# Optimization experiments

Measured on AMD Instinct MI355X. Metric: run time of the kernel, lower is better.

Reference implementation:

```python
import jax, jax.numpy as jnp
import numpy as np

B, N, C, H, D, K = 8, 2000, 64, 64, 16, 2  # batch, nodes, hidden, hidden_hidden, embed_dim, cheb_k


def setup_inputs() -> dict:
    key = jax.random.key(0)
    ks = jax.random.split(key, 12)
    f = lambda k, s, sc=1.0: jax.random.normal(k, s, dtype=jnp.float32) * sc
    return {
        "z": f(ks[0], (B, N, C)),
        "W_in": f(ks[1], (H, C), 0.1),
        "b_in": f(ks[2], (H,), 0.1),
        "W_out": f(ks[3], (C * C, H), 0.05),
        "b_out": f(ks[4], (C * C,), 0.05),
        "emb": f(ks[5], (N, D), 0.1),
        "wp": f(ks[6], (D, K, H, H), 0.1),
        "bp": f(ks[7], (D, H), 0.1),
        "w1": f(ks[8], (C,)),
        "w2": f(ks[9], (C,)),
        "vs": f(ks[10], (N, N), 0.02),
        "bs": f(ks[11], (N, N), 0.02),
    }


def reference(z, W_in, b_in, W_out, b_out, emb, wp, bp, w1, w2, vs, bs):
    # linear_in + relu: (B,N,C) -> (B,N,H)
    h = jax.nn.relu(jnp.einsum("bnc,hc->bnh", z, W_in) + b_in)

    # data-adaptive graph: softmax over rows of relu(emb @ emb^T)
    A = jax.nn.softmax(jax.nn.relu(emb @ emb.T), axis=1)  # (N,N)
    S = jnp.stack([jnp.eye(N, dtype=z.dtype), A], axis=0)  # (K,N,N), cheb_k=2

    # spatial attention on h (x = h.unsqueeze(1), f_in == H == C)
    e1 = h @ w1  # (B,N)
    e2 = h @ w2  # (B,N)
    prod = e1[:, :, None] * e2[:, None, :]  # (B,N,N) outer product
    E = jax.nn.softmax(
        jnp.einsum("nm,bmp->bnp", vs, jax.nn.sigmoid(prod + bs)), axis=-1
    )  # (B,N,N)

    # batched supports: E.unsqueeze(1) @ S -> (B,K,N,N)
    sup = jnp.einsum("bnm,kmp->bknp", E, S)

    # node-adaptive weights / bias
    weights = jnp.einsum("nd,dkio->nkio", emb, wp)  # (N,K,H,H)
    bias = emb @ bp  # (N,H)

    # graph conv
    x_g = jnp.einsum("bknm,bmc->bnkc", sup, h)  # (B,N,K,H)
    g = jnp.einsum("bnki,nkio->bno", x_g, weights) + bias  # (B,N,H)

    # linear_out + view + tanh, scaled by 0.1
    out = jnp.tanh(jnp.einsum("bnh,oh->bno", g, W_out) + b_out)
    return 0.1 * out.reshape(B, N, C, C)
```

## Files before the change

### kernel.cpp

```cpp
#include <hip/hip_runtime.h>
#include <hip/hip_bf16.h>

#define NN 2000
#define NP 2048
#define BB 8
#define HH 64
#define DD 16

typedef __hip_bfloat16 bf16;
typedef short bf16x8 __attribute__((ext_vector_type(8)));
typedef float f32x4 __attribute__((ext_vector_type(4)));

__device__ __forceinline__ float fast_sigmoid(float x) {
    return 1.0f / (1.0f + __expf(-x));
}
__device__ __forceinline__ float fast_tanh(float x) {
    float e = __expf(2.0f * x);
    return 1.0f - 2.0f / (e + 1.0f);
}

__device__ __forceinline__ void glds16(const void* g, void* l) {
    __builtin_amdgcn_global_load_lds(
        (const __attribute__((address_space(1))) void*)g,
        (__attribute__((address_space(3))) void*)l, 16, 0, 0);
}

__global__ __launch_bounds__(256) void k_h(
        const float* __restrict__ z, const float* __restrict__ W_in,
        const float* __restrict__ b_in, const float* __restrict__ w1,
        const float* __restrict__ w2, float* __restrict__ h,
        float* __restrict__ e1, float* __restrict__ e2) {
    __shared__ float WT[64 * 65];
    __shared__ float zs[4][64];
    int t = threadIdx.x;
    int lane = t & 63, ty = t >> 6;
    int bn0 = blockIdx.x * 4;
    for (int i = t; i < 64 * 64; i += 256) {
        int hh = i >> 6, c = i & 63;
        WT[c * 65 + hh] = W_in[i];
    }
    zs[ty][lane] = z[(size_t)(bn0 + ty) * 64 + lane];
    __syncthreads();
    float acc = b_in[lane];
    #pragma unroll
    for (int c = 0; c < 64; c++) acc += zs[ty][c] * WT[c * 65 + lane];
    float hv = fmaxf(acc, 0.0f);
    h[(size_t)(bn0 + ty) * 64 + lane] = hv;
    float p1 = hv * w1[lane], p2 = hv * w2[lane];
    #pragma unroll
    for (int off = 32; off > 0; off >>= 1) {
        p1 += __shfl_down(p1, off);
        p2 += __shfl_down(p2, off);
    }
    if (lane == 0) { e1[bn0 + ty] = p1; e2[bn0 + ty] = p2; }
}

__global__ __launch_bounds__(256) void k_A(const float* __restrict__ emb,
                                           bf16* __restrict__ A) {
    int i = blockIdx.x, t = threadIdx.x;
    if (i >= NN) {
        for (int j = t; j < NP; j += 256) A[(size_t)i * NP + j] = __float2bfloat16(0.0f);
        return;
    }
    __shared__ float ei[DD];
    __shared__ float rowbuf[NP];
    __shared__ float red[256];
    if (t < DD) ei[t] = emb[i * DD + t];
    __syncthreads();
    float lmax = -1e30f;
    for (int j = t; j < NP; j += 256) {
        float s = 0.0f;
        if (j < NN) {
            #pragma unroll
            for (int d = 0; d < DD; d++) s += ei[d] * emb[j * DD + d];
            s = fmaxf(s, 0.0f);
            lmax = fmaxf(lmax, s);
        }
        rowbuf[j] = s;
    }
    red[t] = lmax; __syncthreads();
    for (int o = 128; o > 0; o >>= 1) { if (t < o) red[t] = fmaxf(red[t], red[t + o]); __syncthreads(); }
    float mx = red[0];
    __syncthreads();
    float lsum = 0.0f;
    for (int j = t; j < NN; j += 256) {
        float e = __expf(rowbuf[j] - mx);
        rowbuf[j] = e; lsum += e;
    }
    red[t] = lsum; __syncthreads();
    for (int o = 128; o > 0; o >>= 1) { if (t < o) red[t] += red[t + o]; __syncthreads(); }
    float inv = 1.0f / red[0];
    for (int j = t; j < NP; j += 256)
        A[(size_t)i * NP + j] = __float2bfloat16(j < NN ? rowbuf[j] * inv : 0.0f);
}

__global__ void k_cvt_vs(const float* __restrict__ vs, bf16* __restrict__ out) {
    int id = blockIdx.x * 256 + threadIdx.x;
    int n = id >> 11, m = id & (NP - 1);
    float v = (n < NN && m < NN) ? vs[n * NN + m] : 0.0f;
    out[id] = __float2bfloat16(v);
}

__global__ void k_cvt_wout(const float* __restrict__ W_out, bf16* __restrict__ out) {
    int id = blockIdx.x * 256 + threadIdx.x;
    out[id] = __float2bfloat16(W_out[id]);
}

__global__ __launch_bounds__(256) void k_wn(const float* __restrict__ emb,
                                            const float* __restrict__ wp,
                                            float* __restrict__ Wn_all) {
    __shared__ float embs[128 * 16];
    int t = threadIdx.x;
    int n0 = blockIdx.x * 128;
    int jo = blockIdx.y * 256 + t;
    float wv[16];
    #pragma unroll
    for (int d = 0; d < 16; d++) wv[d] = wp[(size_t)d * 8192 + jo];
    for (int s = t; s < 128 * 16; s += 256) {
        int i = s >> 4, d = s & 15;
        int n = n0 + i;
        embs[s] = (n < NN) ? emb[n * 16 + d] : 0.f;
    }
    __syncthreads();
    for (int i = 0; i < 128; i++) {
        int n = n0 + i;
        if (n >= NN) break;
        const f32x4* ev = (const f32x4*)&embs[i * 16];
        f32x4 e0 = ev[0], e1 = ev[1], e2 = ev[2], e3 = ev[3];
        float a = 0.f;
        #pragma unroll
        for (int q = 0; q < 4; q++) a += e0[q] * wv[q];
        #pragma unroll
        for (int q = 0; q < 4; q++) a += e1[q] * wv[4 + q];
        #pragma unroll
        for (int q = 0; q < 4; q++) a += e2[q] * wv[8 + q];
        #pragma unroll
        for (int q = 0; q < 4; q++) a += e3[q] * wv[12 + q];
        Wn_all[(size_t)n * 8192 + jo] = a;
    }
}

__global__ __launch_bounds__(256) void k_hT(const float* __restrict__ h,
                                            bf16* __restrict__ hTcat,
                                            bf16* __restrict__ hsT) {
    __shared__ float tile[64 * 65];
    int nt = blockIdx.x, b = blockIdx.y;
    int tx = threadIdx.x & 63, ty = threadIdx.x >> 6;
    int n0 = nt * 64;
    for (int i = ty * 16; i < ty * 16 + 16; i++) {
        int n = n0 + i;
        tile[i * 65 + tx] = (n < NN) ? h[((size_t)b * NN + n) * 64 + tx] : 0.0f;
    }
    __syncthreads();
    for (int i = ty * 16; i < ty * 16 + 16; i++) {
        bf16 v = __float2bfloat16(tile[tx * 65 + i]);
        hTcat[((size_t)b * 64 + i) * NP + n0 + tx] = v;
        hsT[((size_t)b * 128 + i) * NP + n0 + tx] = v;
    }
}

__global__ __launch_bounds__(256) void k_AhT(const float* __restrict__ Ahcat,
                                             bf16* __restrict__ hsT) {
    __shared__ float tile[64 * 65];
    int pt = blockIdx.x, b = blockIdx.y;
    int tx = threadIdx.x & 63, ty = threadIdx.x >> 6;
    int p0 = pt * 64, q0 = b * 64;
    for (int i = ty * 16; i < ty * 16 + 16; i++)
        tile[i * 65 + tx] = Ahcat[((size_t)p0 + i) * 512 + q0 + tx];
    __syncthreads();
    for (int i = ty * 16; i < ty * 16 + 16; i++)
        hsT[((size_t)b * 128 + 64 + i) * NP + p0 + tx] =
            __float2bfloat16(tile[tx * 65 + i]);
}

__global__ __launch_bounds__(256) void k_Tt(const float* __restrict__ e1,
                                            const float* __restrict__ e2,
                                            const float* __restrict__ bs,
                                            bf16* __restrict__ Tt) {
    __shared__ float tile[64 * 65];
    int b = blockIdx.z;
    e1 += (size_t)b * NN;
    e2 += (size_t)b * NN;
    Tt += (size_t)b * NP * NP;
    int mt = blockIdx.x, pt = blockIdx.y;
    int tx = threadIdx.x & 63, ty = threadIdx.x >> 6;
    int m0 = mt * 64, p0 = pt * 64;
    int p = p0 + tx;
    float e2v = (p < NN) ? e2[p] : 0.0f;
    for (int i = ty * 16; i < ty * 16 + 16; i++) {
        int m = m0 + i;
        float v = 0.0f;
        if (m < NN && p < NN)
            v = fast_sigmoid(e1[m] * e2v + bs[(size_t)m * NN + p]);
        tile[i * 65 + tx] = v;
    }
    __syncthreads();
    for (int i = ty * 16; i < ty * 16 + 16; i++)
        Tt[((size_t)p0 + i) * NP + m0 + tx] = __float2bfloat16(tile[tx * 65 + i]);
}

__global__ __launch_bounds__(512) void k_gemm256p(
        const bf16* __restrict__ X, const bf16* __restrict__ Yt,
        bf16* __restrict__ P, float* __restrict__ rowsumP,
        int K, int ldx, int ldy,
        long long sY, long long sP) {
    __shared__ short As[2 * 256 * 64];
    __shared__ short Bs[2 * 256 * 64];
    __shared__ float rsum2[4][256];
    int z = blockIdx.z;
    const bf16* Xp = X;
    const bf16* Yp = Yt + (long long)z * sY;
    bf16* Pp = P + (long long)z * sP;
    int tid = threadIdx.x;
    int m0 = blockIdx.x * 256, n0 = blockIdx.y * 256;
    int wave = tid >> 6, lane = tid & 63;
    int wr = wave >> 2, wc = wave & 3;
    int fr = lane & 15, kq = lane >> 4;

    f32x4 zero = {0.f, 0.f, 0.f, 0.f};
    f32x4 acc[8][4];
    #pragma unroll
    for (int i = 0; i < 8; i++)
        #pragma unroll
        for (int j = 0; j < 4; j++) acc[i][j] = zero;

    int r8 = tid >> 3;
    int sslot = (tid & 7) ^ (r8 & 7);
    const bf16* xsrc = Xp + (long long)(m0 + r8) * ldx + sslot * 8;
    const bf16* ysrc = Yp + (long long)(n0 + r8) * ldy + sslot * 8;

    auto STAGE = [&](int tile) {
        short* Ab = As + (tile & 1) * 16384 + tid * 8;
        short* Bb = Bs + (tile & 1) * 16384 + tid * 8;
        int ko = tile * 64;
        #pragma unroll
        for (int c = 0; c < 4; c++) {
            glds16(xsrc + (long long)(c * 64) * ldx + ko, Ab + c * 4096);
            glds16(ysrc + (long long)(c * 64) * ldy + ko, Bb + c * 4096);
        }
    };

    int NT = K >> 6;
    STAGE(0);
    STAGE(1);
    asm volatile("s_waitcnt vmcnt(8)" ::: "memory");
    __builtin_amdgcn_s_barrier();

    for (int t = 0; t < NT; t++) {
        const short* Ab = As + (t & 1) * 16384 + wr * 8192 + fr * 64;
        const short* Bb = Bs + (t & 1) * 16384 + wc * 4096 + fr * 64;
        #pragma unroll
        for (int ks = 0; ks < 2; ks++) {
            int s = ((ks * 4 + kq) ^ (fr & 7)) * 8;
            bf16x8 a[8], b[4];
            #pragma unroll
            for (int i = 0; i < 8; i++)
                a[i] = *(const bf16x8*)(Ab + i * 1024 + s);
            #pragma unroll
            for (int j = 0; j < 4; j++)
                b[j] = *(const bf16x8*)(Bb + j * 1024 + s);
            __builtin_amdgcn_s_setprio(1);
            #pragma unroll
            for (int i = 0; i < 8; i++)
                #pragma unroll
                for (int j = 0; j < 4; j++)
                    acc[i][j] = __builtin_amdgcn_mfma_f32_16x16x32_bf16(a[i], b[j], acc[i][j], 0, 0, 0);
            __builtin_amdgcn_s_setprio(0);
        }
        __builtin_amdgcn_sched_barrier(0);
        __builtin_amdgcn_s_barrier();
        __builtin_amdgcn_sched_barrier(0);
        if (t + 2 < NT) {
            STAGE(t + 2);
            asm volatile("s_waitcnt vmcnt(8)" ::: "memory");
            __builtin_amdgcn_s_barrier();
        } else if (t + 1 < NT) {
            asm volatile("s_waitcnt vmcnt(0)" ::: "memory");
            __builtin_amdgcn_s_barrier();
        }
    }

    int rq = kq * 4;
    #pragma unroll
    for (int i = 0; i < 8; i++) {
        #pragma unroll
        for (int r = 0; r < 4; r++) {
            int lrow = wr * 128 + i * 16 + rq + r;
            long long grow = m0 + lrow;
            float rs = 0.f;
            #pragma unroll
            for (int j = 0; j < 4; j++) {
                int col = n0 + wc * 64 + j * 16 + fr;
                float e = (col < NN) ? __expf(acc[i][j][r]) : 0.f;
                Pp[grow * (long long)NP + col] = __float2bfloat16(e);
                rs += e;
            }
            rs += __shfl_xor(rs, 1);
            rs += __shfl_xor(rs, 2);
            rs += __shfl_xor(rs, 4);
            rs += __shfl_xor(rs, 8);
            if (fr == 0) rsum2[wc][lrow] = rs;
        }
    }
    __syncthreads();
    if (tid < 256) {
        float s = rsum2[0][tid] + rsum2[1][tid] + rsum2[2][tid] + rsum2[3][tid];
        rowsumP[((long long)z * 8 + blockIdx.y) * NP + m0 + tid] = s;
    }
}

template<bool TANH, int KSPLIT>
__global__ __launch_bounds__(256) void k_gemm_bt(
        const bf16* __restrict__ X, const bf16* __restrict__ Yt,
        float* __restrict__ C, const float* __restrict__ bias,
        int K, int ldx, int ldy, int ldc,
        long long sX, long long sY, long long sC, long long sSlice) {
    __shared__ short As[128 * 32];
    __shared__ short Bs[128 * 32];
    int zz = blockIdx.z;
    int ks = 0;
    if (KSPLIT > 1) { ks = zz % KSPLIT; zz /= KSPLIT; }
    const bf16* Xp = X + (long long)zz * sX;
    const bf16* Yp = Yt + (long long)zz * sY;
    float* Cp = C + (long long)zz * sC + (long long)ks * sSlice;
    int tid = threadIdx.x;
    int m0 = blockIdx.x * 128, n0 = blockIdx.y * 128;
    int wave = tid >> 6, lane = tid & 63;
    int wm = (wave >> 1) * 64, wn = (wave & 1) * 64;
    int fr = lane & 15, kq = lane >> 4;

    f32x4 zero = {0.f, 0.f, 0.f, 0.f};
    f32x4 acc[4][4];
    #pragma unroll
    for (int i = 0; i < 4; i++)
        #pragma unroll
        for (int j = 0; j < 4; j++) acc[i][j] = zero;

    int lrow = lane >> 2, lcol = (lane & 3) * 8;
    const bf16* xg0 = Xp + (long long)(m0 + wave * 16 + lrow) * ldx + lcol;
    const bf16* xg1 = xg0 + (long long)64 * ldx;
    const bf16* yg0 = Yp + (long long)(n0 + wave * 16 + lrow) * ldy + lcol;
    const bf16* yg1 = yg0 + (long long)64 * ldy;
    short* lA0 = As + wave * 512;
    short* lA1 = As + (wave + 4) * 512;
    short* lB0 = Bs + wave * 512;
    short* lB1 = Bs + (wave + 4) * 512;

    int kbeg = (KSPLIT > 1) ? ks * (K / KSPLIT) : 0;
    int kend = kbeg + K / KSPLIT;
    for (int k0 = kbeg; k0 < kend; k0 += 32) {
        __syncthreads();
        glds16(xg0 + k0, lA0);
        glds16(xg1 + k0, lA1);
        glds16(yg0 + k0, lB0);
        glds16(yg1 + k0, lB1);
        __syncthreads();
        bf16x8 a[4], b[4];
        #pragma unroll
        for (int i = 0; i < 4; i++)
            a[i] = *(const bf16x8*)(As + (wm + i * 16 + fr) * 32 + kq * 8);
        #pragma unroll
        for (int j = 0; j < 4; j++)
            b[j] = *(const bf16x8*)(Bs + (wn + j * 16 + fr) * 32 + kq * 8);
        #pragma unroll
        for (int i = 0; i < 4; i++)
            #pragma unroll
            for (int j = 0; j < 4; j++)
                acc[i][j] = __builtin_amdgcn_mfma_f32_16x16x32_bf16(a[i], b[j], acc[i][j], 0, 0, 0);
    }
    int rq = kq * 4;
    for (int i = 0; i < 4; i++)
        for (int j = 0; j < 4; j++) {
            int col = n0 + wn + j * 16 + fr;
            float bv = TANH ? bias[col] : 0.0f;
            #pragma unroll
            for (int r = 0; r < 4; r++) {
                int row = m0 + wm + i * 16 + rq + r;
                float v = acc[i][j][r];
                Cp[(long long)row * ldc + col] =
                    TANH ? 0.1f * fast_tanh(v + bv) : v;
            }
        }
}

__global__ __launch_bounds__(256) void k_reduce4(const float* __restrict__ part,
                                                 float* __restrict__ out, int total) {
    int i = (blockIdx.x * 256 + threadIdx.x) * 4;
    f32x4 a = *(const f32x4*)(part + i);
    f32x4 b = *(const f32x4*)(part + (size_t)total + i);
    f32x4 c = *(const f32x4*)(part + (size_t)2 * total + i);
    f32x4 d = *(const f32x4*)(part + (size_t)3 * total + i);
    *(f32x4*)(out + i) = (a + b) + (c + d);
}

__global__ __launch_bounds__(256) void k_g(
        const float* __restrict__ Wn_all, const float* __restrict__ bp,
        const float* __restrict__ emb, const float* __restrict__ xg,
        const float* __restrict__ rowsumP, bf16* __restrict__ gbf) {
    __shared__ float Wn[8192];
    __shared__ float xgs[1024];
    __shared__ float biass[64];
    __shared__ float invs[8];
    int n = blockIdx.x, t = threadIdx.x;
    if (t < 8) {
        float s = 0.f;
        #pragma unroll
        for (int y = 0; y < 8; y++)
            s += rowsumP[((size_t)(t * 8 + y)) * NP + n];
        invs[t] = 1.0f / s;
    }
    if (t >= 64 && t < 128) {
        int o = t - 64;
        float a = 0.f;
        #pragma unroll
        for (int d = 0; d < 16; d++) a += emb[n * 16 + d] * bp[d * 64 + o];
        biass[o] = a;
    }
    {
        const f32x4* src = (const f32x4*)(Wn_all + (size_t)n * 8192);
        f32x4* dst = (f32x4*)Wn;
        #pragma unroll
        for (int s = 0; s < 8; s++) dst[s * 256 + t] = src[s * 256 + t];
    }
    __syncthreads();
    for (int s = 0; s < 4; s++) {
        int id = t + s * 256;
        int b = id >> 7, j = id & 127;
        xgs[id] = xg[((size_t)b * NP + n) * 128 + j] * invs[b];
    }
    __syncthreads();
    int o = t & 63, bh = t >> 6;
    for (int half = 0; half < 2; half++) {
        int b = bh + half * 4;
        float a = biass[o];
        for (int j = 0; j < 128; j++) a += xgs[b * 128 + j] * Wn[j * 64 + o];
        gbf[((size_t)b * NN + n) * 64 + o] = __float2bfloat16(a);
    }
}

extern "C" void kernel_launch(void* const* d_in, const int* in_sizes, int n_in,
                              void* d_out, int out_size, void* d_ws, size_t ws_size,
                              hipStream_t stream) {
    const float* z     = (const float*)d_in[0];
    const float* W_in  = (const float*)d_in[1];
    const float* b_in  = (const float*)d_in[2];
    const float* W_out = (const float*)d_in[3];
    const float* b_out = (const float*)d_in[4];
    const float* emb   = (const float*)d_in[5];
    const float* wp    = (const float*)d_in[6];
    const float* bp    = (const float*)d_in[7];
    const float* w1    = (const float*)d_in[8];
    const float* w2    = (const float*)d_in[9];
    const float* vs    = (const float*)d_in[10];
    const float* bs    = (const float*)d_in[11];

    char* p = (char*)d_ws;
    auto alloc = [&](size_t bytes) -> char* {
        char* r = p;
        p += (bytes + 255) & ~(size_t)255;
        return r;
    };
    float* h       = (float*)alloc((size_t)BB * NN * 64 * 4);
    float* e1      = (float*)alloc((size_t)BB * NN * 4);
    float* e2      = (float*)alloc((size_t)BB * NN * 4);
    bf16*  A_bf    = (bf16*) alloc((size_t)NP * NP * 2);
    bf16*  vs_bf   = (bf16*) alloc((size_t)NP * NP * 2);
    bf16*  Tt_all  = (bf16*) alloc((size_t)BB * NP * NP * 2);
    bf16*  P_all   = (bf16*) alloc((size_t)BB * NP * NP * 2);
    float* rowsumP = (float*)alloc((size_t)BB * 8 * NP * 4);
    bf16*  hTcat   = (bf16*) alloc((size_t)512 * NP * 2);
    float* Ahcat   = (float*)alloc((size_t)NP * 512 * 4);
    float* AhPart  = (float*)alloc((size_t)4 * NP * 512 * 4);
    bf16*  hsT     = (bf16*) alloc((size_t)BB * 128 * NP * 2);
    float* xg      = (float*)alloc((size_t)BB * NP * 128 * 4);
    float* xgPart  = (float*)alloc((size_t)4 * BB * NP * 128 * 4);
    bf16*  gbf     = (bf16*) alloc((size_t)BB * NN * 64 * 2);
    bf16*  Wo_bf   = (bf16*) alloc((size_t)4096 * 64 * 2);
    float* Wn_all  = (float*)alloc((size_t)NN * 8192 * 4);

    k_h<<<BB * NN / 4, 256, 0, stream>>>(z, W_in, b_in, w1, w2, h, e1, e2);
    k_A<<<NP, 256, 0, stream>>>(emb, A_bf);
    k_cvt_vs<<<(NP * NP) / 256, 256, 0, stream>>>(vs, vs_bf);
    k_cvt_wout<<<(4096 * 64) / 256, 256, 0, stream>>>(W_out, Wo_bf);
    k_wn<<<dim3(16, 32), 256, 0, stream>>>(emb, wp, Wn_all);
    k_hT<<<dim3(NP / 64, BB), 256, 0, stream>>>(h, hTcat, hsT);

    k_gemm_bt<false, 4><<<dim3(16, 4, 4), 256, 0, stream>>>(
        A_bf, hTcat, AhPart, nullptr, NP, NP, NP, 512,
        0, 0, 0, (long long)NP * 512);
    k_reduce4<<<(NP * 512) / 1024, 256, 0, stream>>>(AhPart, Ahcat, NP * 512);
    k_AhT<<<dim3(NP / 64, BB), 256, 0, stream>>>(Ahcat, hsT);

    k_Tt<<<dim3(NP / 64, NP / 64, BB), 256, 0, stream>>>(e1, e2, bs, Tt_all);
    k_gemm256p<<<dim3(8, 8, BB), 512, 0, stream>>>(
        vs_bf, Tt_all, P_all, rowsumP, NP, NP, NP,
        (long long)NP * NP, (long long)NP * NP);

    k_gemm_bt<false, 4><<<dim3(16, 1, BB * 4), 256, 0, stream>>>(
        P_all, hsT, xgPart, nullptr, NP, NP, NP, 128,
        (long long)NP * NP, (long long)128 * NP, (long long)NP * 128,
        (long long)BB * NP * 128);
    k_reduce4<<<(BB * NP * 128) / 1024, 256, 0, stream>>>(xgPart, xg, BB * NP * 128);

    k_g<<<NN, 256, 0, stream>>>(Wn_all, bp, emb, xg, rowsumP, gbf);
    k_gemm_bt<true, 1><<<dim3(125, 32, 1), 256, 0, stream>>>(
        gbf, Wo_bf, (float*)d_out, b_out, 64, 64, 64, 4096, 0, 0, 0, 0);
}
```

Measured before the change: 646.8 us.

## Fuse softmax-numerator GEMM with P·h GEMM via LDS-resident exp tile

The vs·T GEMM epilogue now writes the exponentiated tile into shared memory instead of global P, then immediately multiplies it by the batch's hsT slice to produce per-column-block partials of x_g. This removes the full bf16 P round trip and one GEMM launch. In exchange it writes 8 fp32 partial slabs that need an 8-way reduction, and expands row-sum partials to 32 per row. The hsT operand is read directly from global memory without staging.

After: 646.5 us. Within noise of the previous version (-0.0%).

```diff
diff --git a/kernel.cpp b/kernel.cpp
--- a/kernel.cpp
+++ b/kernel.cpp
@@ -199,18 +199,17 @@
         Tt[((size_t)p0 + i) * NP + m0 + tx] = __float2bfloat16(tile[tx * 65 + i]);
 }
 
-__global__ __launch_bounds__(512) void k_gemm256p(
+__global__ __launch_bounds__(512) void k_gemm256pv(
         const bf16* __restrict__ X, const bf16* __restrict__ Yt,
-        bf16* __restrict__ P, float* __restrict__ rowsumP,
-        int K, int ldx, int ldy,
-        long long sY, long long sP) {
-    __shared__ short As[2 * 256 * 64];
-    __shared__ short Bs[2 * 256 * 64];
-    __shared__ float rsum2[4][256];
+        const bf16* __restrict__ hsT, float* __restrict__ xgPart,
+        float* __restrict__ rsPart,
+        int K, int ldx, int ldy, long long sY, long long sHs) {
+    __shared__ short LDSb[65536];
+    short* Asb = LDSb;
+    short* Bsb = LDSb + 32768;
     int z = blockIdx.z;
     const bf16* Xp = X;
     const bf16* Yp = Yt + (long long)z * sY;
-    bf16* Pp = P + (long long)z * sP;
     int tid = threadIdx.x;
     int m0 = blockIdx.x * 256, n0 = blockIdx.y * 256;
     int wave = tid >> 6, lane = tid & 63;
@@ -230,8 +229,8 @@
     const bf16* ysrc = Yp + (long long)(n0 + r8) * ldy + sslot * 8;
 
     auto STAGE = [&](int tile) {
-        short* Ab = As + (tile & 1) * 16384 + tid * 8;
-        short* Bb = Bs + (tile & 1) * 16384 + tid * 8;
+        short* Ab = Asb + (tile & 1) * 16384 + tid * 8;
+        short* Bb = Bsb + (tile & 1) * 16384 + tid * 8;
         int ko = tile * 64;
         #pragma unroll
         for (int c = 0; c < 4; c++) {
@@ -247,8 +246,8 @@
     __builtin_amdgcn_s_barrier();
 
     for (int t = 0; t < NT; t++) {
-        const short* Ab = As + (t & 1) * 16384 + wr * 8192 + fr * 64;
-        const short* Bb = Bs + (t & 1) * 16384 + wc * 4096 + fr * 64;
+        const short* Ab = Asb + (t & 1) * 16384 + wr * 8192 + fr * 64;
+        const short* Bb = Bsb + (t & 1) * 16384 + wc * 4096 + fr * 64;
         #pragma unroll
         for (int ks = 0; ks < 2; ks++) {
             int s = ((ks * 4 + kq) ^ (fr & 7)) * 8;
@@ -286,27 +285,64 @@
         #pragma unroll
         for (int r = 0; r < 4; r++) {
             int lrow = wr * 128 + i * 16 + rq + r;
-            long long grow = m0 + lrow;
             float rs = 0.f;
             #pragma unroll
             for (int j = 0; j < 4; j++) {
-                int col = n0 + wc * 64 + j * 16 + fr;
-                float e = (col < NN) ? __expf(acc[i][j][r]) : 0.f;
-                Pp[grow * (long long)NP + col] = __float2bfloat16(e);
+                int lcol = wc * 64 + j * 16 + fr;
+                float e = (n0 + lcol < NN) ? __expf(acc[i][j][r]) : 0.f;
+                bf16 bv = __float2bfloat16(e);
+                int sl = (lcol >> 3) ^ (lrow & 7);
+                LDSb[lrow * 256 + sl * 8 + (lcol & 7)] = *(short*)&bv;
                 rs += e;
             }
             rs += __shfl_xor(rs, 1);
             rs += __shfl_xor(rs, 2);
             rs += __shfl_xor(rs, 4);
             rs += __shfl_xor(rs, 8);
-            if (fr == 0) rsum2[wc][lrow] = rs;
-        }
-    }
-    __syncthreads();
-    if (tid < 256) {
-        float s = rsum2[0][tid] + rsum2[1][tid] + rsum2[2][tid] + rsum2[3][tid];
-        rowsumP[((long long)z * 8 + blockIdx.y) * NP + m0 + tid] = s;
-    }
+            if (fr == 0)
+                rsPart[((long long)z * 32 + blockIdx.y * 4 + wc) * NP + m0 + lrow] = rs;
+        }
+    }
+    __syncthreads();
+
+    const bf16* hz = hsT + (long long)z * sHs;
+    int wr2 = wave >> 2, wc2 = wave & 3;
+    f32x4 acc2[8][2];
+    #pragma unroll
+    for (int i = 0; i < 8; i++)
+        #pragma unroll
+        for (int jj = 0; jj < 2; jj++) acc2[i][jj] = zero;
+    #pragma unroll
+    for (int ks = 0; ks < 8; ks++) {
+        bf16x8 a2[8], b2[2];
+        #pragma unroll
+        for (int i = 0; i < 8; i++) {
+            int row = wr2 * 128 + i * 16 + fr;
+            int sl = (ks * 4 + kq) ^ (row & 7);
+            a2[i] = *(const bf16x8*)(LDSb + row * 256 + sl * 8);
+        }
+        #pragma unroll
+        for (int jj = 0; jj < 2; jj++)
+            b2[jj] = *(const bf16x8*)(hz + (long long)(wc2 * 32 + jj * 16 + fr) * NP
+                                      + n0 + ks * 32 + kq * 8);
+        #pragma unroll
+        for (int i = 0; i < 8; i++)
+            #pragma unroll
+            for (int jj = 0; jj < 2; jj++)
+                acc2[i][jj] = __builtin_amdgcn_mfma_f32_16x16x32_bf16(a2[i], b2[jj], acc2[i][jj], 0, 0, 0);
+    }
+    long long slab = (long long)blockIdx.y * ((long long)BB * NP * 128);
+    #pragma unroll
+    for (int i = 0; i < 8; i++)
+        #pragma unroll
+        for (int jj = 0; jj < 2; jj++) {
+            int jcol = wc2 * 32 + jj * 16 + fr;
+            #pragma unroll
+            for (int r = 0; r < 4; r++) {
+                int n = m0 + wr2 * 128 + i * 16 + rq + r;
+                xgPart[slab + ((long long)z * NP + n) * 128 + jcol] = acc2[i][jj][r];
+            }
+        }
 }
 
 template<bool TANH, int KSPLIT>
@@ -393,10 +429,20 @@
     *(f32x4*)(out + i) = (a + b) + (c + d);
 }
 
+__global__ __launch_bounds__(256) void k_reduce8(const float* __restrict__ part,
+                                                 float* __restrict__ out, int total) {
+    int i = (blockIdx.x * 256 + threadIdx.x) * 4;
+    f32x4 s = *(const f32x4*)(part + i);
+    #pragma unroll
+    for (int k = 1; k < 8; k++)
+        s += *(const f32x4*)(part + (size_t)k * total + i);
+    *(f32x4*)(out + i) = s;
+}
+
 __global__ __launch_bounds__(256) void k_g(
         const float* __restrict__ Wn_all, const float* __restrict__ bp,
         const float* __restrict__ emb, const float* __restrict__ xg,
-        const float* __restrict__ rowsumP, bf16* __restrict__ gbf) {
+        const float* __restrict__ rsPart, bf16* __restrict__ gbf) {
     __shared__ float Wn[8192];
     __shared__ float xgs[1024];
     __shared__ float biass[64];
@@ -405,8 +451,8 @@
     if (t < 8) {
         float s = 0.f;
         #pragma unroll
-        for (int y = 0; y < 8; y++)
-            s += rowsumP[((size_t)(t * 8 + y)) * NP + n];
+        for (int y = 0; y < 32; y++)
+            s += rsPart[((size_t)t * 32 + y) * NP + n];
         invs[t] = 1.0f / s;
     }
     if (t >= 64 && t < 128) {
@@ -466,14 +512,13 @@
     bf16*  A_bf    = (bf16*) alloc((size_t)NP * NP * 2);
     bf16*  vs_bf   = (bf16*) alloc((size_t)NP * NP * 2);
     bf16*  Tt_all  = (bf16*) alloc((size_t)BB * NP * NP * 2);
-    bf16*  P_all   = (bf16*) alloc((size_t)BB * NP * NP * 2);
-    float* rowsumP = (float*)alloc((size_t)BB * 8 * NP * 4);
+    float* rsPart  = (float*)alloc((size_t)BB * 32 * NP * 4);
     bf16*  hTcat   = (bf16*) alloc((size_t)512 * NP * 2);
     float* Ahcat   = (float*)alloc((size_t)NP * 512 * 4);
     float* AhPart  = (float*)alloc((size_t)4 * NP * 512 * 4);
     bf16*  hsT     = (bf16*) alloc((size_t)BB * 128 * NP * 2);
     float* xg      = (float*)alloc((size_t)BB * NP * 128 * 4);
-    float* xgPart  = (float*)alloc((size_t)4 * BB * NP * 128 * 4);
+    float* xgPart8 = (float*)alloc((size_t)8 * BB * NP * 128 * 4);
     bf16*  gbf     = (bf16*) alloc((size_t)BB * NN * 64 * 2);
     bf16*  Wo_bf   = (bf16*) alloc((size_t)4096 * 64 * 2);
     float* Wn_all  = (float*)alloc((size_t)NN * 8192 * 4);
@@ -492,17 +537,12 @@
     k_AhT<<<dim3(NP / 64, BB), 256, 0, stream>>>(Ahcat, hsT);
 
     k_Tt<<<dim3(NP / 64, NP / 64, BB), 256, 0, stream>>>(e1, e2, bs, Tt_all);
-    k_gemm256p<<<dim3(8, 8, BB), 512, 0, stream>>>(
-        vs_bf, Tt_all, P_all, rowsumP, NP, NP, NP,
-        (long long)NP * NP, (long long)NP * NP);
-
-    k_gemm_bt<false, 4><<<dim3(16, 1, BB * 4), 256, 0, stream>>>(
-        P_all, hsT, xgPart, nullptr, NP, NP, NP, 128,
-        (long long)NP * NP, (long long)128 * NP, (long long)NP * 128,
-        (long long)BB * NP * 128);
-    k_reduce4<<<(BB * NP * 128) / 1024, 256, 0, stream>>>(xgPart, xg, BB * NP * 128);
-
-    k_g<<<NN, 256, 0, stream>>>(Wn_all, bp, emb, xg, rowsumP, gbf);
+    k_gemm256pv<<<dim3(8, 8, BB), 512, 0, stream>>>(
+        vs_bf, Tt_all, hsT, xgPart8, rsPart, NP, NP, NP,
+        (long long)NP * NP, (long long)128 * NP);
+    k_reduce8<<<(BB * NP * 128) / 1024, 256, 0, stream>>>(xgPart8, xg, BB * NP * 128);
+
+    k_g<<<NN, 256, 0, stream>>>(Wn_all, bp, emb, xg, rsPart, gbf);
     k_gemm_bt<true, 1><<<dim3(125, 32, 1), 256, 0, stream>>>(
         gbf, Wo_bf, (float*)d_out, b_out, 64, 64, 64, 4096, 0, 0, 0, 0);
 }
```
